# Kernel tuning notes

Hardware: AMD Instinct MI355X
Metric: run time of the kernel (lower is better)

## Reference

```python
import jax, jax.numpy as jnp
import numpy as np

D_MODEL = 1024
NUM_HEADS = 16
D_K = D_MODEL // NUM_HEADS


def setup_inputs() -> dict:
    key = jax.random.key(0)
    ks = jax.random.split(key, 9)
    s = 1.0 / np.sqrt(D_MODEL)
    inp = {
        "x": jax.random.normal(ks[0], (4, 2048, D_MODEL), dtype=jnp.float32),
        "W_q": jax.random.uniform(ks[1], (D_MODEL, D_MODEL), jnp.float32, -s, s),
        "b_q": jax.random.uniform(ks[2], (D_MODEL,), jnp.float32, -s, s),
        "W_k": jax.random.uniform(ks[3], (D_MODEL, D_MODEL), jnp.float32, -s, s),
        "b_k": jax.random.uniform(ks[4], (D_MODEL,), jnp.float32, -s, s),
        "W_v": jax.random.uniform(ks[5], (D_MODEL, D_MODEL), jnp.float32, -s, s),
        "b_v": jax.random.uniform(ks[6], (D_MODEL,), jnp.float32, -s, s),
        "W_o": jax.random.uniform(ks[7], (D_MODEL, D_MODEL), jnp.float32, -s, s),
        "b_o": jax.random.uniform(ks[8], (D_MODEL,), jnp.float32, -s, s),
    }
    return inp


def reference(x, W_q, b_q, W_k, b_k, W_v, b_v, W_o, b_o):
    B, S, _ = x.shape
    # Linear layers (torch convention: y = x @ W.T + b), split into heads -> [B, H, S, d_k]
    def proj(W, b):
        y = jnp.einsum("bsd,ed->bse", x, W) + b
        return y.reshape(B, S, NUM_HEADS, D_K).transpose(0, 2, 1, 3)

    Q = proj(W_q, b_q)
    K = proj(W_k, b_k)
    V = proj(W_v, b_v)

    scale = 1.0 / jnp.sqrt(jnp.asarray(D_K, dtype=x.dtype))
    scores = jnp.einsum("bhqd,bhkd->bhqk", Q, K) * scale  # [B, H, S, S]
    attn = jax.nn.softmax(scores, axis=-1)
    out = jnp.einsum("bhqk,bhkd->bhqd", attn, V)  # [B, H, S, d_k]
    out = out.transpose(0, 2, 1, 3).reshape(B, S, D_MODEL)
    return jnp.einsum("bsd,ed->bse", out, W_o) + b_o
```

## Files before the change

### kernel.cpp

```cpp
#include <hip/hip_runtime.h>
#include <hip/hip_bf16.h>
#include <math.h>


constexpr int D = 1024;
constexpr int H = 16;
constexpr int DK = 64;
constexpr int PSTR = 72;

typedef unsigned short u16;
typedef __attribute__((ext_vector_type(8))) short v8s;
typedef __attribute__((ext_vector_type(4))) float v4f;
typedef const __attribute__((address_space(1))) void gvoid;
typedef __attribute__((address_space(3))) void lvoid;
typedef __attribute__((address_space(3))) u16 ls_u16;
typedef __attribute__((address_space(3))) v8s lv8s;

__device__ __forceinline__ u16 rne_bf16(float f) {
  unsigned u = __float_as_uint(f);
  u += 0x7FFFu + ((u >> 16) & 1u);
  return (u16)(u >> 16);
}

__device__ __forceinline__ unsigned pk_bf16(float a, float b) {
  __hip_bfloat162 t = __float22bfloat162_rn(float2{a, b});
  return *reinterpret_cast<unsigned*>(&t);
}

__global__ __launch_bounds__(256) void split_kernel(
    const float* __restrict__ in, u16* __restrict__ hi, u16* __restrict__ lo, int n4)
{
  const int i = blockIdx.x * 256 + threadIdx.x;
  if (i >= n4) return;
  const float4 v = ((const float4*)in)[i];
  const float f[4] = {v.x, v.y, v.z, v.w};
  ushort4 h, l;
  u16 hh[4], ll[4];
#pragma unroll
  for (int j = 0; j < 4; ++j) {
    const unsigned u = __float_as_uint(f[j]);
    hh[j] = (u16)(u >> 16);
    const float hf = __uint_as_float(u & 0xFFFF0000u);
    ll[j] = rne_bf16(f[j] - hf);
  }
  h.x = hh[0]; h.y = hh[1]; h.z = hh[2]; h.w = hh[3];
  l.x = ll[0]; l.y = ll[1]; l.z = ll[2]; l.w = ll[3];
  ((ushort4*)hi)[i] = h;
  ((ushort4*)lo)[i] = l;
}

template<int R>
__device__ __forceinline__ void stage_arr(const u16* __restrict__ src, ls_u16* dst,
                                          int tid, int row0, int k0)
{
  const int cg = (tid & 3) ^ ((tid >> 3) & 3);
#pragma unroll
  for (int j = 0; j < R / 128; ++j) {
    const int row = j * 128 + (tid >> 2);
    __builtin_amdgcn_global_load_lds(
        (gvoid*)(src + (size_t)(row0 + row) * D + k0 + cg * 8),
        (lvoid*)(dst + j * 4096 + tid * 8), 16, 0, 0);
  }
}

__device__ __forceinline__ void cfence() { asm volatile("" ::: "memory"); }

template<int BM, int BN, int EPI>
__global__ __launch_bounds__(512, 2) void gemm_pipe_kernel(
    const u16* __restrict__ Ahi, const u16* __restrict__ Alo,
    const u16* __restrict__ Whi, const u16* __restrict__ Wlo,
    const float* __restrict__ b0v, const float* __restrict__ b1v, const float* __restrict__ b2v,
    u16* __restrict__ Qb, u16* __restrict__ Kb, u16* __restrict__ Vtb,
    float* __restrict__ C, int S_)
{
  constexpr int TA = BM * 32;
  constexpr int TB = BN * 32;
  constexpr int BUFSZ = 2 * TA + 2 * TB;
  __shared__ u16 lds[3][BUFSZ];

  const int tid = threadIdx.x;
  const int lane = tid & 63, w = tid >> 6;
  const int wm = (w >> 1) * 64, wn = (w & 1) * 64;
  const int fr = lane & 15, fq = lane >> 4;
  const int csw = (fq ^ ((fr >> 1) & 3)) * 8;

  const int gx = gridDim.x;
  const int gyd = gridDim.y;
  const int nwg = gx * gyd;
  int id = blockIdx.y * gx + blockIdx.x;
  id = (id & 7) * (nwg >> 3) + (id >> 3);
  constexpr int GM = 4;
  const int per_grp = GM * gyd;
  const int grp = id / per_grp;
  const int ing = id - grp * per_grp;
  const int m0 = (grp * GM + (ing & (GM - 1))) * BM;
  const int n0 = (ing / GM) * BN;

  v4f acc[4][4];
#pragma unroll
  for (int mi = 0; mi < 4; ++mi)
#pragma unroll
    for (int ni = 0; ni < 4; ++ni) acc[mi][ni] = (v4f){0.f, 0.f, 0.f, 0.f};

  ls_u16* pb0 = (ls_u16*)&lds[0][0];
  ls_u16* pb1 = (ls_u16*)&lds[1][0];
  ls_u16* pb2 = (ls_u16*)&lds[2][0];

  int aoff[4], boff[4];
#pragma unroll
  for (int i = 0; i < 4; ++i) {
    aoff[i] = (wm + i * 16 + fr) * 32 + csw;
    boff[i] = 2 * TA + (wn + i * 16 + fr) * 32 + csw;
  }

#pragma unroll
  for (int p = 0; p < 2; ++p) {
    ls_u16* pb = (p == 0) ? pb0 : pb1;
    stage_arr<BM>(Ahi, pb, tid, m0, p * 32);
    stage_arr<BM>(Alo, pb + TA, tid, m0, p * 32);
    stage_arr<BN>(Whi, pb + 2 * TA, tid, n0, p * 32);
    stage_arr<BN>(Wlo, pb + 2 * TA + TB, tid, n0, p * 32);
  }

#pragma unroll 2
  for (int k = 0; k < 32; ++k) {
    const int ks = (k + 2 < 32) ? (k + 2) * 32 : 31 * 32;

    asm volatile("s_waitcnt vmcnt(6)" ::: "memory");
    __builtin_amdgcn_s_barrier();
    cfence();

    v8s ah[4], bh[4], tf[4];
#pragma unroll
    for (int i = 0; i < 4; ++i) ah[i] = *(const lv8s*)(pb0 + aoff[i]);
#pragma unroll
    for (int i = 0; i < 4; ++i) bh[i] = *(const lv8s*)(pb0 + boff[i]);
    stage_arr<BM>(Ahi, pb2, tid, m0, ks);
    __builtin_amdgcn_s_setprio(1);
#pragma unroll
    for (int mi = 0; mi < 4; ++mi)
#pragma unroll
      for (int ni = 0; ni < 4; ++ni)
        acc[mi][ni] = __builtin_amdgcn_mfma_f32_16x16x32_bf16(ah[mi], bh[ni], acc[mi][ni], 0, 0, 0);
    __builtin_amdgcn_s_setprio(0);
    cfence();
    __builtin_amdgcn_s_barrier();
    cfence();

#pragma unroll
    for (int i = 0; i < 4; ++i) tf[i] = *(const lv8s*)(pb0 + TA + aoff[i]);
    stage_arr<BM>(Alo, pb2 + TA, tid, m0, ks);
    __builtin_amdgcn_s_setprio(1);
#pragma unroll
    for (int mi = 0; mi < 4; ++mi)
#pragma unroll
      for (int ni = 0; ni < 4; ++ni)
        acc[mi][ni] = __builtin_amdgcn_mfma_f32_16x16x32_bf16(tf[mi], bh[ni], acc[mi][ni], 0, 0, 0);
    __builtin_amdgcn_s_setprio(0);
    cfence();
    __builtin_amdgcn_s_barrier();
    cfence();

#pragma unroll
    for (int i = 0; i < 4; ++i) tf[i] = *(const lv8s*)(pb0 + boff[i] + TB);
    stage_arr<BN>(Whi, pb2 + 2 * TA, tid, n0, ks);
    stage_arr<BN>(Wlo, pb2 + 2 * TA + TB, tid, n0, ks);
    __builtin_amdgcn_s_setprio(1);
#pragma unroll
    for (int mi = 0; mi < 4; ++mi)
#pragma unroll
      for (int ni = 0; ni < 4; ++ni)
        acc[mi][ni] = __builtin_amdgcn_mfma_f32_16x16x32_bf16(ah[mi], tf[ni], acc[mi][ni], 0, 0, 0);
    __builtin_amdgcn_s_setprio(0);
    cfence();

    ls_u16* t = pb0; pb0 = pb1; pb1 = pb2; pb2 = t;
  }

  const int lane4 = fq * 4;
  if constexpr (EPI == 0) {
    const int wsel = n0 >> 10;
    const float* bias = (wsel == 0) ? b0v : (wsel == 1) ? b1v : b2v;
    u16* Cb = (wsel == 0) ? Qb : (wsel == 1) ? Kb : Vtb;
    const int bb = m0 / S_;
    const int s0 = m0 - bb * S_;
#pragma unroll
    for (int mi = 0; mi < 4; ++mi) {
#pragma unroll
      for (int ni = 0; ni < 4; ++ni) {
        const int n = n0 + wn + ni * 16 + fr;
        const int nl = n & (D - 1);
        const float bvv = bias[nl];
        const int h = nl >> 6, dk = nl & 63;
#pragma unroll
        for (int r = 0; r < 4; ++r) {
          const int s = s0 + wm + mi * 16 + lane4 + r;
          const float val = acc[mi][ni][r] + bvv;
          if (wsel < 2)
            Cb[((size_t)(bb * H + h) * S_ + s) * DK + dk] = rne_bf16(val);
          else
            Cb[((size_t)(bb * H + h) * DK + dk) * S_ + s] = rne_bf16(val);
        }
      }
    }
  } else {
#pragma unroll
    for (int mi = 0; mi < 4; ++mi)
#pragma unroll
      for (int ni = 0; ni < 4; ++ni) {
        const int n = n0 + wn + ni * 16 + fr;
        const float bvv = b0v[n];
#pragma unroll
        for (int r = 0; r < 4; ++r) {
          const int m = m0 + wm + mi * 16 + lane4 + r;
          C[(size_t)m * D + n] = acc[mi][ni][r] + bvv;
        }
      }
  }
}

__global__ __launch_bounds__(256) void attn_mfma_kernel(
    const u16* __restrict__ Qb, const u16* __restrict__ Kb, const u16* __restrict__ Vtb,
    u16* __restrict__ Ohi, u16* __restrict__ Olo, int S_)
{
  __shared__ u16 Ks[64 * 64];
  __shared__ u16 Vt[64 * 64];
  __shared__ u16 Pl[4][32 * PSTR];

  const int tid = threadIdx.x;
  const int lane = tid & 63, w = tid >> 6;
  const int fr = lane & 15, fq = lane >> 4;
  const int q0 = blockIdx.x * 128;
  const int h = blockIdx.y, b = blockIdx.z;
  const int wq = w * 32;
  const size_t base = (size_t)(b * H + h) * S_ * DK;

  const int srow = tid >> 3;
  const int scb = (tid & 7) ^ (srow & 7);

  v8s qa[2][2];
#pragma unroll
  for (int ni = 0; ni < 2; ++ni)
#pragma unroll
    for (int ks = 0; ks < 2; ++ks)
      qa[ni][ks] = *(const v8s*)(Qb + base + (size_t)(q0 + wq + ni * 16 + fr) * DK + ks * 32 + fq * 8);

  v4f o[4][2];
  float lsum[2] = {0.f, 0.f};
#pragma unroll
  for (int mi = 0; mi < 4; ++mi)
#pragma unroll
    for (int ni = 0; ni < 2; ++ni) o[mi][ni] = (v4f){0.f, 0.f, 0.f, 0.f};

  for (int j0 = 0; j0 < S_; j0 += 64) {
    __syncthreads();
#pragma unroll
    for (int rep = 0; rep < 2; ++rep) {
      const int row = rep * 32 + srow;
      const int ldso = rep * 2048 + tid * 8;
      __builtin_amdgcn_global_load_lds((gvoid*)(Kb + base + (size_t)(j0 + row) * DK + scb * 8),
                                       (lvoid*)(Ks + ldso), 16, 0, 0);
      __builtin_amdgcn_global_load_lds((gvoid*)(Vtb + base + (size_t)row * S_ + j0 + scb * 8),
                                       (lvoid*)(Vt + ldso), 16, 0, 0);
    }
    __syncthreads();

    v4f s[4][2];
#pragma unroll
    for (int mi = 0; mi < 4; ++mi)
#pragma unroll
      for (int ni = 0; ni < 2; ++ni) s[mi][ni] = (v4f){0.f, 0.f, 0.f, 0.f};
#pragma unroll
    for (int ks = 0; ks < 2; ++ks) {
      v8s kb[4];
#pragma unroll
      for (int mi = 0; mi < 4; ++mi) {
        const int row = mi * 16 + fr;
        kb[mi] = *(const v8s*)&Ks[row * 64 + (((ks * 4 + fq) ^ (row & 7)) * 8)];
      }
#pragma unroll
      for (int mi = 0; mi < 4; ++mi)
#pragma unroll
        for (int ni = 0; ni < 2; ++ni)
          s[mi][ni] = __builtin_amdgcn_mfma_f32_16x16x32_bf16(kb[mi], qa[ni][ks], s[mi][ni], 0, 0, 0);
    }

#pragma unroll
    for (int mi = 0; mi < 4; ++mi)
#pragma unroll
      for (int ni = 0; ni < 2; ++ni) {
        float p[4];
#pragma unroll
        for (int r = 0; r < 4; ++r) p[r] = __expf(s[mi][ni][r] * 0.125f);
        lsum[ni] += (p[0] + p[1]) + (p[2] + p[3]);
        uint2 pk;
        pk.x = pk_bf16(p[0], p[1]);
        pk.y = pk_bf16(p[2], p[3]);
        *(uint2*)&Pl[w][(ni * 16 + fr) * PSTR + mi * 16 + fq * 4] = pk;
      }

#pragma unroll
    for (int ks = 0; ks < 2; ++ks) {
      v8s vb[4], pa[2];
#pragma unroll
      for (int mi = 0; mi < 4; ++mi) {
        const int row = mi * 16 + fr;
        vb[mi] = *(const v8s*)&Vt[row * 64 + (((ks * 4 + fq) ^ (row & 7)) * 8)];
      }
#pragma unroll
      for (int ni = 0; ni < 2; ++ni)
        pa[ni] = *(const v8s*)&Pl[w][(ni * 16 + fr) * PSTR + ks * 32 + fq * 8];
#pragma unroll
      for (int mi = 0; mi < 4; ++mi)
#pragma unroll
        for (int ni = 0; ni < 2; ++ni)
          o[mi][ni] = __builtin_amdgcn_mfma_f32_16x16x32_bf16(vb[mi], pa[ni], o[mi][ni], 0, 0, 0);
    }
  }

  float linv[2];
#pragma unroll
  for (int ni = 0; ni < 2; ++ni) {
    float l = lsum[ni];
    l += __shfl_xor(l, 16);
    l += __shfl_xor(l, 32);
    linv[ni] = 1.f / l;
  }

#pragma unroll
  for (int ni = 0; ni < 2; ++ni) {
    const int q = q0 + wq + ni * 16 + fr;
    const size_t rowbase = (size_t)(b * S_ + q) * D + h * DK;
#pragma unroll
    for (int mi = 0; mi < 4; ++mi) {
      const int d0 = mi * 16 + fq * 4;
      float v[4];
      unsigned u[4];
      float res[4];
#pragma unroll
      for (int r = 0; r < 4; ++r) {
        v[r] = o[mi][ni][r] * linv[ni];
        u[r] = __float_as_uint(v[r]);
        res[r] = v[r] - __uint_as_float(u[r] & 0xFFFF0000u);
      }
      uint2 hi, lo;
      hi.x = (u[1] & 0xFFFF0000u) | (u[0] >> 16);
      hi.y = (u[3] & 0xFFFF0000u) | (u[2] >> 16);
      lo.x = pk_bf16(res[0], res[1]);
      lo.y = pk_bf16(res[2], res[3]);
      *(uint2*)(Ohi + rowbase + d0) = hi;
      *(uint2*)(Olo + rowbase + d0) = lo;
    }
  }
}

extern "C" void kernel_launch(void* const* d_in, const int* in_sizes, int n_in,
                              void* d_out, int out_size, void* d_ws, size_t ws_size,
                              hipStream_t stream) {
  const float* x  = (const float*)d_in[0];
  const float* Wq = (const float*)d_in[1];
  const float* bq = (const float*)d_in[2];
  const float* Wk = (const float*)d_in[3];
  const float* bk = (const float*)d_in[4];
  const float* Wv = (const float*)d_in[5];
  const float* bv = (const float*)d_in[6];
  const float* Wo = (const float*)d_in[7];
  const float* bo = (const float*)d_in[8];

  const int M = in_sizes[0] / D;
  const int B = 4;
  const int S_ = M / B;
  const size_t MD = (size_t)M * D;
  const size_t DD = (size_t)D * D;

  u16* Qb    = (u16*)d_ws;
  u16* Kb    = Qb + MD;
  u16* Vtb   = Kb + MD;
  u16* xs_hi = Vtb + MD;
  u16* xs_lo = xs_hi + MD;
  u16* Ohi   = xs_lo + MD;
  u16* Olo   = Ohi + MD;
  u16* wo_hi = Olo + MD;
  u16* wo_lo = wo_hi + DD;

  u16* wqkv_hi = (u16*)d_out;
  u16* wqkv_lo = wqkv_hi + 3 * DD;

  const int gx = (int)(MD / 4 / 256);
  const int gw = (int)(DD / 4 / 256);

  split_kernel<<<gx, 256, 0, stream>>>(x,  xs_hi, xs_lo, (int)(MD / 4));
  split_kernel<<<gw, 256, 0, stream>>>(Wq, wqkv_hi,          wqkv_lo,          (int)(DD / 4));
  split_kernel<<<gw, 256, 0, stream>>>(Wk, wqkv_hi + DD,     wqkv_lo + DD,     (int)(DD / 4));
  split_kernel<<<gw, 256, 0, stream>>>(Wv, wqkv_hi + 2 * DD, wqkv_lo + 2 * DD, (int)(DD / 4));
  split_kernel<<<gw, 256, 0, stream>>>(Wo, wo_hi, wo_lo, (int)(DD / 4));

  dim3 gq(M / 256, 3 * D / 128);
  gemm_pipe_kernel<256, 128, 0><<<gq, 512, 0, stream>>>(
      xs_hi, xs_lo, wqkv_hi, wqkv_lo, bq, bk, bv, Qb, Kb, Vtb, nullptr, S_);

  dim3 ga(S_ / 128, H, B);
  attn_mfma_kernel<<<ga, 256, 0, stream>>>(Qb, Kb, Vtb, Ohi, Olo, S_);

  dim3 go(M / 256, D / 128);
  gemm_pipe_kernel<256, 128, 1><<<go, 512, 0, stream>>>(
      Ohi, Olo, wo_hi, wo_lo, bo, nullptr, nullptr, nullptr, nullptr, nullptr,
      (float*)d_out, S_);
}
```

Measured before the change: 440.5 us.

## Double-buffer K/V tiles in attention and merge weight split launches

The attention kernel now keeps two LDS buffers for K and V tiles. It prefetches the next tile with global_load_lds while the MFMA work runs on the current one, and needs only one waitcnt and barrier per iteration instead of two syncthreads. The four weight split launches are merged into a single 2D-grid launch to cut launch overhead. The extra LDS buffers raise shared memory per block, which may reduce occupancy.

```diff
diff --git a/kernel.cpp b/kernel.cpp
--- a/kernel.cpp
+++ b/kernel.cpp
@@ -27,11 +27,12 @@
   return *reinterpret_cast<unsigned*>(&t);
 }
 
-__global__ __launch_bounds__(256) void split_kernel(
-    const float* __restrict__ in, u16* __restrict__ hi, u16* __restrict__ lo, int n4)
-{
-  const int i = blockIdx.x * 256 + threadIdx.x;
-  if (i >= n4) return;
+__device__ __forceinline__ void cfence() { asm volatile("" ::: "memory"); }
+
+__device__ __forceinline__ void split_body(const float* __restrict__ in,
+                                           u16* __restrict__ hi, u16* __restrict__ lo,
+                                           int i)
+{
   const float4 v = ((const float4*)in)[i];
   const float f[4] = {v.x, v.y, v.z, v.w};
   ushort4 h, l;
@@ -49,6 +50,30 @@
   ((ushort4*)lo)[i] = l;
 }
 
+__global__ __launch_bounds__(256) void split_kernel(
+    const float* __restrict__ in, u16* __restrict__ hi, u16* __restrict__ lo, int n4)
+{
+  const int i = blockIdx.x * 256 + threadIdx.x;
+  if (i >= n4) return;
+  split_body(in, hi, lo, i);
+}
+
+__global__ __launch_bounds__(256) void splitw_kernel(
+    const float* __restrict__ w0, const float* __restrict__ w1,
+    const float* __restrict__ w2, const float* __restrict__ w3,
+    u16* __restrict__ qkv_hi, u16* __restrict__ qkv_lo,
+    u16* __restrict__ o_hi, u16* __restrict__ o_lo, int n4)
+{
+  const int i = blockIdx.x * 256 + threadIdx.x;
+  if (i >= n4) return;
+  const int y = blockIdx.y;
+  const float* src = (y == 0) ? w0 : (y == 1) ? w1 : (y == 2) ? w2 : w3;
+  const size_t off = (size_t)y * (size_t)n4;
+  u16* hi = (y < 3) ? qkv_hi + off * 4 : o_hi;
+  u16* lo = (y < 3) ? qkv_lo + off * 4 : o_lo;
+  split_body(src, hi, lo, i);
+}
+
 template<int R>
 __device__ __forceinline__ void stage_arr(const u16* __restrict__ src, ls_u16* dst,
                                           int tid, int row0, int k0)
@@ -62,8 +87,6 @@
         (lvoid*)(dst + j * 4096 + tid * 8), 16, 0, 0);
   }
 }
-
-__device__ __forceinline__ void cfence() { asm volatile("" ::: "memory"); }
 
 template<int BM, int BN, int EPI>
 __global__ __launch_bounds__(512, 2) void gemm_pipe_kernel(
@@ -223,8 +246,8 @@
     const u16* __restrict__ Qb, const u16* __restrict__ Kb, const u16* __restrict__ Vtb,
     u16* __restrict__ Ohi, u16* __restrict__ Olo, int S_)
 {
-  __shared__ u16 Ks[64 * 64];
-  __shared__ u16 Vt[64 * 64];
+  __shared__ u16 Ks[2][64 * 64];
+  __shared__ u16 Vt[2][64 * 64];
   __shared__ u16 Pl[4][32 * PSTR];
 
   const int tid = threadIdx.x;
@@ -238,32 +261,45 @@
   const int srow = tid >> 3;
   const int scb = (tid & 7) ^ (srow & 7);
 
-  v8s qa[2][2];
-#pragma unroll
-  for (int ni = 0; ni < 2; ++ni)
-#pragma unroll
-    for (int ks = 0; ks < 2; ++ks)
-      qa[ni][ks] = *(const v8s*)(Qb + base + (size_t)(q0 + wq + ni * 16 + fr) * DK + ks * 32 + fq * 8);
-
-  v4f o[4][2];
-  float lsum[2] = {0.f, 0.f};
-#pragma unroll
-  for (int mi = 0; mi < 4; ++mi)
-#pragma unroll
-    for (int ni = 0; ni < 2; ++ni) o[mi][ni] = (v4f){0.f, 0.f, 0.f, 0.f};
-
-  for (int j0 = 0; j0 < S_; j0 += 64) {
-    __syncthreads();
+  auto stage_kv = [&](int j0, int bufi) {
 #pragma unroll
     for (int rep = 0; rep < 2; ++rep) {
       const int row = rep * 32 + srow;
       const int ldso = rep * 2048 + tid * 8;
       __builtin_amdgcn_global_load_lds((gvoid*)(Kb + base + (size_t)(j0 + row) * DK + scb * 8),
-                                       (lvoid*)(Ks + ldso), 16, 0, 0);
+                                       (lvoid*)(&Ks[bufi][0] + ldso), 16, 0, 0);
       __builtin_amdgcn_global_load_lds((gvoid*)(Vtb + base + (size_t)row * S_ + j0 + scb * 8),
-                                       (lvoid*)(Vt + ldso), 16, 0, 0);
+                                       (lvoid*)(&Vt[bufi][0] + ldso), 16, 0, 0);
     }
-    __syncthreads();
+  };
+
+  stage_kv(0, 0);
+
+  v8s qa[2][2];
+#pragma unroll
+  for (int ni = 0; ni < 2; ++ni)
+#pragma unroll
+    for (int ks = 0; ks < 2; ++ks)
+      qa[ni][ks] = *(const v8s*)(Qb + base + (size_t)(q0 + wq + ni * 16 + fr) * DK + ks * 32 + fq * 8);
+
+  v4f o[4][2];
+  float lsum[2] = {0.f, 0.f};
+#pragma unroll
+  for (int mi = 0; mi < 4; ++mi)
+#pragma unroll
+    for (int ni = 0; ni < 2; ++ni) o[mi][ni] = (v4f){0.f, 0.f, 0.f, 0.f};
+
+  asm volatile("s_waitcnt vmcnt(0)" ::: "memory");
+  __builtin_amdgcn_s_barrier();
+  cfence();
+
+  const int NT = S_ >> 6;
+  for (int jt = 0; jt < NT; ++jt) {
+    const int cur = jt & 1;
+    if (jt + 1 < NT) stage_kv((jt + 1) * 64, cur ^ 1);
+
+    const u16* Kc = &Ks[cur][0];
+    const u16* Vc = &Vt[cur][0];
 
     v4f s[4][2];
 #pragma unroll
@@ -276,7 +312,7 @@
 #pragma unroll
       for (int mi = 0; mi < 4; ++mi) {
         const int row = mi * 16 + fr;
-        kb[mi] = *(const v8s*)&Ks[row * 64 + (((ks * 4 + fq) ^ (row & 7)) * 8)];
+        kb[mi] = *(const v8s*)&Kc[row * 64 + (((ks * 4 + fq) ^ (row & 7)) * 8)];
       }
 #pragma unroll
       for (int mi = 0; mi < 4; ++mi)
@@ -305,7 +341,7 @@
 #pragma unroll
       for (int mi = 0; mi < 4; ++mi) {
         const int row = mi * 16 + fr;
-        vb[mi] = *(const v8s*)&Vt[row * 64 + (((ks * 4 + fq) ^ (row & 7)) * 8)];
+        vb[mi] = *(const v8s*)&Vc[row * 64 + (((ks * 4 + fq) ^ (row & 7)) * 8)];
       }
 #pragma unroll
       for (int ni = 0; ni < 2; ++ni)
@@ -316,6 +352,11 @@
         for (int ni = 0; ni < 2; ++ni)
           o[mi][ni] = __builtin_amdgcn_mfma_f32_16x16x32_bf16(vb[mi], pa[ni], o[mi][ni], 0, 0, 0);
     }
+
+    asm volatile("s_waitcnt vmcnt(0)" ::: "memory");
+    cfence();
+    __builtin_amdgcn_s_barrier();
+    cfence();
   }
 
   float linv[2];
@@ -389,11 +430,10 @@
   const int gx = (int)(MD / 4 / 256);
   const int gw = (int)(DD / 4 / 256);
 
-  split_kernel<<<gx, 256, 0, stream>>>(x,  xs_hi, xs_lo, (int)(MD / 4));
-  split_kernel<<<gw, 256, 0, stream>>>(Wq, wqkv_hi,          wqkv_lo,          (int)(DD / 4));
-  split_kernel<<<gw, 256, 0, stream>>>(Wk, wqkv_hi + DD,     wqkv_lo + DD,     (int)(DD / 4));
-  split_kernel<<<gw, 256, 0, stream>>>(Wv, wqkv_hi + 2 * DD, wqkv_lo + 2 * DD, (int)(DD / 4));
-  split_kernel<<<gw, 256, 0, stream>>>(Wo, wo_hi, wo_lo, (int)(DD / 4));
+  split_kernel<<<gx, 256, 0, stream>>>(x, xs_hi, xs_lo, (int)(MD / 4));
+  dim3 gws(gw, 4);
+  splitw_kernel<<<gws, 256, 0, stream>>>(Wq, Wk, Wv, Wo, wqkv_hi, wqkv_lo,
+                                         wo_hi, wo_lo, (int)(DD / 4));
 
   dim3 gq(M / 256, 3 * D / 128);
   gemm_pipe_kernel<256, 128, 0><<<gq, 512, 0, stream>>>(
```

Result: faster. 430.1 us (-2.4%).
